# Kernel tuning notes

Hardware: AMD Instinct MI355X
Metric: run time of the kernel (lower is better)

The kernel has to match this reference:

```python
import jax, jax.numpy as jnp
import numpy as np

# module config (mirrors init_kwargs)
D_MODEL = 1024
N_HEADS = 16
HEAD_DIM = D_MODEL // N_HEADS
WINDOW = 512
PREFIX = 16
B = 2
S = 4096  # divisible by WINDOW; S > WINDOW + PREFIX -> chunked windowed path


def setup_inputs() -> dict:
    key = jax.random.key(0)
    k1, k2, k3 = jax.random.split(key, 3)
    x = jax.random.normal(k1, (B, S, D_MODEL), dtype=jnp.float32)
    w_qkv = jax.random.normal(k2, (3 * D_MODEL, D_MODEL), dtype=jnp.float32) * 0.02
    w_out = jax.random.normal(k3, (D_MODEL, D_MODEL), dtype=jnp.float32) * 0.02
    return {"x": x, "w_qkv": w_qkv, "w_out": w_out}


def _windowed_global_attention(q, k, v):
    """q,k,v: [B,H,S,Dh]. Causal sliding-window (WINDOW) + global prefix (PREFIX) attention.
    Exactly matches torch's chunked SDPA: for query chunk starting at q_start, allowed keys are
    k_pos < PREFIX (causal) plus local keys in (q_pos-WINDOW, q_pos] with k_pos >= PREFIX."""
    Bb, H, S_, Dh = q.shape
    W, P = WINDOW, PREFIX
    C = S_ // W  # number of query chunks
    scale = 1.0 / np.sqrt(Dh).astype(np.float32)

    qc = q.reshape(Bb, H, C, W, Dh)  # [B,H,C,W,Dh]
    # pad W zero-keys at front so every chunk gathers a uniform 2W-key local tail
    kp = jnp.pad(k, ((0, 0), (0, 0), (W, 0), (0, 0)))
    vp = jnp.pad(v, ((0, 0), (0, 0), (W, 0), (0, 0)))
    tail_idx = jnp.arange(C)[:, None] * W + jnp.arange(2 * W)[None, :]  # [C,2W] (padded coords)
    kt = kp[:, :, tail_idx, :]  # [B,H,C,2W,Dh]
    vt = vp[:, :, tail_idx, :]
    kg = k[:, :, :P, :]  # global prefix keys [B,H,P,Dh]
    vg = v[:, :, :P, :]

    sg = jnp.einsum('bhcqd,bhkd->bhcqk', qc, kg) * scale   # [B,H,C,W,P]
    st = jnp.einsum('bhcqd,bhckd->bhcqk', qc, kt) * scale  # [B,H,C,W,2W]

    q_pos = jnp.arange(C)[:, None] * W + jnp.arange(W)[None, :]          # [C,W]
    kt_pos = jnp.arange(C)[:, None] * W - W + jnp.arange(2 * W)[None, :]  # [C,2W]
    # global prefix: causal only
    mg = jnp.arange(P)[None, None, :] <= q_pos[:, :, None]                # [C,W,P]
    # local tail: causal & within window & not already covered by global prefix (and not padding)
    diff = q_pos[:, :, None] - kt_pos[:, None, :]                          # [C,W,2W]
    mt = (diff >= 0) & (diff < W) & (kt_pos[:, None, :] >= P)

    neg = jnp.asarray(-1e9, sg.dtype)
    scores = jnp.concatenate([
        jnp.where(mg[None, None], sg, neg),
        jnp.where(mt[None, None], st, neg),
    ], axis=-1)  # [B,H,C,W,P+2W]
    attn = jax.nn.softmax(scores, axis=-1)

    vcat = jnp.concatenate([
        jnp.broadcast_to(vg[:, :, None], (Bb, H, C, P, Dh)), vt
    ], axis=3)  # [B,H,C,P+2W,Dh]
    out = jnp.einsum('bhcqk,bhckd->bhcqd', attn, vcat)
    return out.reshape(Bb, H, S_, Dh)


def reference(x, w_qkv, w_out):
    Bb, S_, Dm = x.shape
    qkv = x @ w_qkv.T                      # [B,S,3*Dm]
    q, k, v = jnp.split(qkv, 3, axis=-1)
    def heads(t):
        return t.reshape(Bb, S_, N_HEADS, HEAD_DIM).transpose(0, 2, 1, 3)
    q, k, v = heads(q), heads(k), heads(v)  # [B,H,S,Dh]
    o = _windowed_global_attention(q, k, v)
    o = o.transpose(0, 2, 1, 3).reshape(Bb, S_, Dm)
    return o @ w_out.T
```

## Files before the change

kernel.cpp:

```cpp
#include <hip/hip_runtime.h>
#include <hip/hip_bf16.h>

#define AS1 __attribute__((address_space(1)))
#define AS3 __attribute__((address_space(3)))

typedef unsigned short u16;
typedef short bf16x8 __attribute__((ext_vector_type(8)));
typedef unsigned short u16x8 __attribute__((ext_vector_type(8)));
typedef float f32x4 __attribute__((ext_vector_type(4)));

#define MFMA16 __builtin_amdgcn_mfma_f32_16x16x32_bf16


__device__ __forceinline__ u16 f2bf(float f) {
  union { float f; unsigned u; } c; c.f = f;
  unsigned u = c.u;
  u = u + 0x7fffu + ((u >> 16) & 1u);
  return (u16)(u >> 16);
}

__device__ __forceinline__ u16 f2bf_trunc(float f) {
  union { float f; unsigned u; } c; c.f = f;
  return (u16)(c.u >> 16);
}

__device__ __forceinline__ void gl_lds16(const void* g, void* l) {
  __builtin_amdgcn_global_load_lds((const AS1 void*)g, (AS3 void*)l, 16, 0, 0);
}


__global__ void cast_all_kernel(const float* __restrict__ x,
                                const float* __restrict__ wqkv,
                                const float* __restrict__ wout,
                                u16* __restrict__ ws) {
  int i = blockIdx.x * blockDim.x + threadIdx.x;
  const float4* src;
  int rel;
  size_t matbase;
  if (i < 2097152)      { src = (const float4*)x + i;                rel = i;           matbase = 0; }
  else if (i < 2883584) { src = (const float4*)wqkv + (i - 2097152); rel = i - 2097152; matbase = 8388608; }
  else                  { src = (const float4*)wout + (i - 2883584); rel = i - 2883584; matbase = 11534336; }
  float4 f = *src;
  ushort4 o;
  o.x = f2bf(f.x); o.y = f2bf(f.y); o.z = f2bf(f.z); o.w = f2bf(f.w);
  int fe  = rel * 4;
  int row = fe >> 10, c = fe & 1023;
  int newc = (c & ~63) | (((((c >> 3) ^ row) & 7) << 3)) | (c & 7);
  ((ushort4*)ws)[(matbase + (size_t)row * 1024 + newc) >> 2] = o;
}


template<int EPI>
__global__ __launch_bounds__(256) void gemm_bt(
    const u16* __restrict__ A, const u16* __restrict__ Bm,
    float* __restrict__ Cf,
    u16* __restrict__ qd, u16* __restrict__ kd, u16* __restrict__ vd,
    int M, int N, int K)
{
  __shared__ u16 As[128 * 64];
  __shared__ u16 Bs[128 * 64];

  const int tid  = threadIdx.x;
  const int wave = tid >> 6, lane = tid & 63;
  const int quad = lane >> 4, l16 = lane & 15;
  const int bm = blockIdx.y * 128, bn = blockIdx.x * 128;
  const int wm = (wave >> 1) * 64, wn = (wave & 1) * 64;

  f32x4 acc[4][4] = {};

  const int srow = wave * 32 + (lane >> 3);
  const int scol = (lane & 7) * 8;

  for (int kt = 0; kt < K; kt += 64) {
    __syncthreads();
    #pragma unroll
    for (int i = 0; i < 4; ++i) {
      gl_lds16(&A[(size_t)(bm + srow + i * 8) * K + kt + scol], &As[(wave * 32 + i * 8) * 64]);
      gl_lds16(&Bm[(size_t)(bn + srow + i * 8) * K + kt + scol], &Bs[(wave * 32 + i * 8) * 64]);
    }
    __syncthreads();
    #pragma unroll
    for (int kk = 0; kk < 64; kk += 32) {
      bf16x8 af[4], bb[4];
      #pragma unroll
      for (int i = 0; i < 4; ++i) {
        int row = wm + i * 16 + l16;
        af[i] = *(const bf16x8*)&As[row * 64 + (((((kk >> 3) + quad) ^ row) & 7) << 3)];
      }
      #pragma unroll
      for (int j = 0; j < 4; ++j) {
        int row = wn + j * 16 + l16;
        bb[j] = *(const bf16x8*)&Bs[row * 64 + (((((kk >> 3) + quad) ^ row) & 7) << 3)];
      }
      #pragma unroll
      for (int i = 0; i < 4; ++i)
        #pragma unroll
        for (int j = 0; j < 4; ++j)
          acc[i][j] = MFMA16(af[i], bb[j], acc[i][j], 0, 0, 0);
    }
  }

  #pragma unroll
  for (int i = 0; i < 4; ++i) {
    #pragma unroll
    for (int j = 0; j < 4; ++j) {
      #pragma unroll
      for (int r = 0; r < 4; ++r) {
        int m = bm + wm + i * 16 + quad * 4 + r;
        int n = bn + wn + j * 16 + l16;
        float val = acc[i][j][r];
        if (EPI == 0) {
          Cf[(size_t)m * N + n] = val;
        } else {
          int part = n >> 10, rem = n & 1023;
          int h = rem >> 6, d = rem & 63;
          int b = m >> 12, s = m & 4095;
          if (part == 0) val *= 0.1803368801111244f;
          u16* dst = (part == 0) ? qd : (part == 1) ? kd : vd;
          dst[((size_t)((b * 16 + h) * 4096 + s)) * 64 + d] = f2bf(val);
        }
      }
    }
  }
}


__global__ __launch_bounds__(256) void transpose_v(const u16* __restrict__ vb,
                                                   u16* __restrict__ vt) {
  __shared__ u16 Lt[64 * 72];
  const int tid = threadIdx.x, bid = blockIdx.x;
  const int bh = bid & 31, st = (bid >> 5) << 6;
  const size_t base = (size_t)bh << 18;
  #pragma unroll
  for (int c = 0; c < 2; ++c) {
    int idx = tid * 8 + c * 2048;
    int row = idx >> 6, col = idx & 63;
    u16x8 vv = *(const u16x8*)&vb[base + (size_t)(st + row) * 64 + col];
    #pragma unroll
    for (int s = 0; s < 8; ++s) Lt[(col + s) * 72 + row] = vv[s];
  }
  __syncthreads();
  #pragma unroll
  for (int c = 0; c < 2; ++c) {
    int d = (tid >> 3) + c * 32;
    int sg = (tid & 7) * 8;
    u16x8 o;
    #pragma unroll
    for (int s = 0; s < 8; ++s) o[s] = Lt[d * 72 + sg + s];
    *(u16x8*)&vt[base + (size_t)d * 4096 + st + sg] = o;
  }
}


__global__ __launch_bounds__(64) void attn_kernel(
    const u16* __restrict__ qb, const u16* __restrict__ kb,
    const u16* __restrict__ vt, u16* __restrict__ ob)
{
  __shared__ u16 Ps[32 * 64];

  const int lane = threadIdx.x;
  const int quad = lane >> 4, l16 = lane & 15;
  const int bid  = blockIdx.x;
  const int bh   = bid & 31;
  const int t0   = (bid >> 5) << 5;
  const size_t base = (size_t)bh << 18;

  bf16x8 aq[2][2];
  #pragma unroll
  for (int i = 0; i < 2; ++i) {
    const u16* qrow = qb + base + (size_t)(t0 + i * 16 + l16) * 64;
    aq[i][0] = *(const bf16x8*)(qrow + quad * 8);
    aq[i][1] = *(const bf16x8*)(qrow + 32 + quad * 8);
  }

  f32x4 oacc[2][4] = {};
  f32x4 lacc[2] = {};
  bf16x8 ones;
  #pragma unroll
  for (int s = 0; s < 8; ++s) ones[s] = (short)0x3F80;

  {
    const u16* krow = kb + base + (size_t)l16 * 64;
    bf16x8 bk0 = *(const bf16x8*)(krow + quad * 8);
    bf16x8 bk1 = *(const bf16x8*)(krow + 32 + quad * 8);
    #pragma unroll
    for (int i = 0; i < 2; ++i) {
      f32x4 t4 = {};
      t4 = MFMA16(aq[i][0], bk0, t4, 0, 0, 0);
      t4 = MFMA16(aq[i][1], bk1, t4, 0, 0, 0);
      #pragma unroll
      for (int r = 0; r < 4; ++r) {
        int qpos = t0 + i * 16 + quad * 4 + r;
        float v = (l16 <= qpos) ? t4[r] : -1e30f;
        float p = exp2f(v);
        int row = i * 16 + quad * 4 + r;
        int gp = ((l16 >> 3) ^ row) & 7;
        Ps[row * 64 + (gp << 3) + (l16 & 7)] = f2bf_trunc(p);
        int gz = ((2 + (l16 >> 3)) ^ row) & 7;
        Ps[row * 64 + (gz << 3) + (l16 & 7)] = 0;
      }
    }
    bf16x8 ap[2];
    #pragma unroll
    for (int i = 0; i < 2; ++i) {
      int rowp = i * 16 + l16;
      int gb = (quad ^ rowp) & 7;
      ap[i] = *(const bf16x8*)&Ps[rowp * 64 + (gb << 3)];
      lacc[i] = MFMA16(ap[i], ones, lacc[i], 0, 0, 0);
    }
    #pragma unroll
    for (int jd = 0; jd < 4; ++jd) {
      const u16* vrow = vt + base + (size_t)(jd * 16 + l16) * 4096;
      bf16x8 bv0 = *(const bf16x8*)(vrow + quad * 8);
      #pragma unroll
      for (int i = 0; i < 2; ++i)
        oacc[i][jd] = MFMA16(ap[i], bv0, oacc[i][jd], 0, 0, 0);
    }
  }

  const int lo = max(0, t0 - 511) >> 6;
  const int hi = (t0 + 31) >> 6;

  for (int t = lo; t <= hi; ++t) {
    const int kb0 = t << 6;
    const bool full = (kb0 >= 16) && (kb0 + 63 <= t0) && (kb0 >= t0 + 31 - 511);

    #pragma unroll
    for (int j = 0; j < 4; ++j) {
      const u16* krow = kb + base + (size_t)(kb0 + j * 16 + l16) * 64;
      bf16x8 bk0 = *(const bf16x8*)(krow + quad * 8);
      bf16x8 bk1 = *(const bf16x8*)(krow + 32 + quad * 8);
      #pragma unroll
      for (int i = 0; i < 2; ++i) {
        f32x4 t4 = {};
        t4 = MFMA16(aq[i][0], bk0, t4, 0, 0, 0);
        t4 = MFMA16(aq[i][1], bk1, t4, 0, 0, 0);
        #pragma unroll
        for (int r = 0; r < 4; ++r) {
          float v = t4[r];
          if (!full) {
            int kpos = kb0 + j * 16 + l16;
            int qpos = t0 + i * 16 + quad * 4 + r;
            int diff = qpos - kpos;
            bool ok = (diff >= 0) && (diff < 512) && (kpos >= 16);
            v = ok ? v : -1e30f;
          }
          float p = exp2f(v);
          int row = i * 16 + quad * 4 + r;
          int gp = ((2 * j + (l16 >> 3)) ^ row) & 7;
          Ps[row * 64 + (gp << 3) + (l16 & 7)] = f2bf_trunc(p);
        }
      }
    }

    bf16x8 ap[2][2];
    #pragma unroll
    for (int i = 0; i < 2; ++i) {
      int rowp = i * 16 + l16;
      int gb = (quad ^ rowp) & 7;
      ap[i][0] = *(const bf16x8*)&Ps[rowp * 64 + (gb << 3)];
      ap[i][1] = *(const bf16x8*)&Ps[rowp * 64 + ((gb ^ 4) << 3)];
      lacc[i] = MFMA16(ap[i][0], ones, lacc[i], 0, 0, 0);
      lacc[i] = MFMA16(ap[i][1], ones, lacc[i], 0, 0, 0);
    }
    #pragma unroll
    for (int jd = 0; jd < 4; ++jd) {
      const u16* vrow = vt + base + (size_t)(jd * 16 + l16) * 4096 + kb0;
      bf16x8 bv0 = *(const bf16x8*)(vrow + quad * 8);
      bf16x8 bv1 = *(const bf16x8*)(vrow + 32 + quad * 8);
      #pragma unroll
      for (int i = 0; i < 2; ++i) {
        oacc[i][jd] = MFMA16(ap[i][0], bv0, oacc[i][jd], 0, 0, 0);
        oacc[i][jd] = MFMA16(ap[i][1], bv1, oacc[i][jd], 0, 0, 0);
      }
    }
  }

  const int b = bh >> 4, h = bh & 15;
  #pragma unroll
  for (int i = 0; i < 2; ++i) {
    #pragma unroll
    for (int r = 0; r < 4; ++r) {
      float inv = 1.f / lacc[i][r];
      int srow = t0 + i * 16 + quad * 4 + r;
      size_t rowoff = ((size_t)(b * 4096 + srow)) * 1024 + h * 64;
      #pragma unroll
      for (int jd = 0; jd < 4; ++jd) {
        int g = ((jd * 2 + (l16 >> 3)) ^ srow) & 7;
        ob[rowoff + (g << 3) + (l16 & 7)] = f2bf(oacc[i][jd][r] * inv);
      }
    }
  }
}


extern "C" void kernel_launch(void* const* d_in, const int* in_sizes, int n_in,
                              void* d_out, int out_size, void* d_ws, size_t ws_size,
                              hipStream_t stream) {
  const float* x    = (const float*)d_in[0];
  const float* wqkv = (const float*)d_in[1];
  const float* wout = (const float*)d_in[2];
  float* out = (float*)d_out;

  u16* ws    = (u16*)d_ws;
  u16* xb    = ws;
  u16* wqkvb = xb + (size_t)8192 * 1024;
  u16* woutb = wqkvb + (size_t)3072 * 1024;
  u16* qbuf  = woutb + (size_t)1024 * 1024;
  u16* kbuf  = qbuf + (size_t)8388608;
  u16* vbuf  = kbuf + (size_t)8388608;
  u16* vtb   = vbuf + (size_t)8388608;
  u16* obuf  = xb;

  cast_all_kernel<<<12288, 256, 0, stream>>>(x, wqkv, wout, ws);

  gemm_bt<1><<<dim3(24, 64), 256, 0, stream>>>(xb, wqkvb, nullptr, qbuf, kbuf, vbuf,
                                               8192, 3072, 1024);
  transpose_v<<<2048, 256, 0, stream>>>(vbuf, vtb);
  attn_kernel<<<4096, 64, 0, stream>>>(qbuf, kbuf, vtb, obuf);
  gemm_bt<0><<<dim3(8, 64), 256, 0, stream>>>(obuf, woutb, out, nullptr, nullptr, nullptr,
                                              8192, 1024, 1024);
}
```

Baseline: 270.3 us.

## Double-buffer K fragments and transpose QK MFMA for packed P stores

Swaps the MFMA operand order so each lane holds four consecutive key scores for one query row. That lets the probabilities be packed into 64-bit LDS stores instead of scalar 16-bit writes, with a new XOR swizzle. K fragments for the next 64-key tile are prefetched into a second register buffer while the current tile computes, to hide global load latency. This costs extra VGPRs and a manually unrolled two-tile loop.

```diff
diff --git a/kernel.cpp b/kernel.cpp
--- a/kernel.cpp
+++ b/kernel.cpp
@@ -19,14 +19,11 @@
   return (u16)(u >> 16);
 }
 
-__device__ __forceinline__ u16 f2bf_trunc(float f) {
-  union { float f; unsigned u; } c; c.f = f;
-  return (u16)(c.u >> 16);
-}
-
 __device__ __forceinline__ void gl_lds16(const void* g, void* l) {
   __builtin_amdgcn_global_load_lds((const AS1 void*)g, (AS3 void*)l, 16, 0, 0);
 }
+
+union fpu { float f; unsigned u; };
 
 
 __global__ void cast_all_kernel(const float* __restrict__ x,
@@ -165,12 +162,12 @@
   const int t0   = (bid >> 5) << 5;
   const size_t base = (size_t)bh << 18;
 
-  bf16x8 aq[2][2];
+  bf16x8 bq[2][2];
   #pragma unroll
   for (int i = 0; i < 2; ++i) {
     const u16* qrow = qb + base + (size_t)(t0 + i * 16 + l16) * 64;
-    aq[i][0] = *(const bf16x8*)(qrow + quad * 8);
-    aq[i][1] = *(const bf16x8*)(qrow + 32 + quad * 8);
+    bq[i][0] = *(const bf16x8*)(qrow + quad * 8);
+    bq[i][1] = *(const bf16x8*)(qrow + 32 + quad * 8);
   }
 
   f32x4 oacc[2][4] = {};
@@ -179,100 +176,117 @@
   #pragma unroll
   for (int s = 0; s < 8; ++s) ones[s] = (short)0x3F80;
 
+  const int lo = max(0, t0 - 511) >> 6;
+  const int hi = (t0 + 31) >> 6;
+
+  auto loadK = [&](int kb0, bf16x8 (&kf)[4][2]) {
+    #pragma unroll
+    for (int j = 0; j < 4; ++j) {
+      const u16* krow = kb + base + (size_t)(kb0 + j * 16 + l16) * 64;
+      kf[j][0] = *(const bf16x8*)(krow + quad * 8);
+      kf[j][1] = *(const bf16x8*)(krow + 32 + quad * 8);
+    }
+  };
+
+  bf16x8 ka[4][2], kbuf2[4][2];
+
   {
     const u16* krow = kb + base + (size_t)l16 * 64;
-    bf16x8 bk0 = *(const bf16x8*)(krow + quad * 8);
-    bf16x8 bk1 = *(const bf16x8*)(krow + 32 + quad * 8);
+    bf16x8 pk0 = *(const bf16x8*)(krow + quad * 8);
+    bf16x8 pk1 = *(const bf16x8*)(krow + 32 + quad * 8);
+    loadK(lo << 6, ka);
+
     #pragma unroll
     for (int i = 0; i < 2; ++i) {
       f32x4 t4 = {};
-      t4 = MFMA16(aq[i][0], bk0, t4, 0, 0, 0);
-      t4 = MFMA16(aq[i][1], bk1, t4, 0, 0, 0);
+      t4 = MFMA16(pk0, bq[i][0], t4, 0, 0, 0);
+      t4 = MFMA16(pk1, bq[i][1], t4, 0, 0, 0);
+      int row = i * 16 + l16;
+      int qpos = t0 + row;
+      fpu p[4];
       #pragma unroll
       for (int r = 0; r < 4; ++r) {
-        int qpos = t0 + i * 16 + quad * 4 + r;
-        float v = (l16 <= qpos) ? t4[r] : -1e30f;
-        float p = exp2f(v);
-        int row = i * 16 + quad * 4 + r;
-        int gp = ((l16 >> 3) ^ row) & 7;
-        Ps[row * 64 + (gp << 3) + (l16 & 7)] = f2bf_trunc(p);
-        int gz = ((2 + (l16 >> 3)) ^ row) & 7;
-        Ps[row * 64 + (gz << 3) + (l16 & 7)] = 0;
-      }
-    }
-    bf16x8 ap[2];
+        int kpos = quad * 4 + r;
+        p[r].f = exp2f(kpos <= qpos ? t4[r] : -1e30f);
+      }
+      uint2 w;
+      w.x = (p[1].u & 0xffff0000u) | (p[0].u >> 16);
+      w.y = (p[3].u & 0xffff0000u) | (p[2].u >> 16);
+      *(uint2*)&Ps[row * 64 + ((quad ^ l16) & 15) * 4] = w;
+      uint2 z = {0u, 0u};
+      *(uint2*)&Ps[row * 64 + (((4 + quad) ^ l16) & 15) * 4] = z;
+    }
     #pragma unroll
     for (int i = 0; i < 2; ++i) {
-      int rowp = i * 16 + l16;
-      int gb = (quad ^ rowp) & 7;
-      ap[i] = *(const bf16x8*)&Ps[rowp * 64 + (gb << 3)];
-      lacc[i] = MFMA16(ap[i], ones, lacc[i], 0, 0, 0);
-    }
-    #pragma unroll
-    for (int jd = 0; jd < 4; ++jd) {
-      const u16* vrow = vt + base + (size_t)(jd * 16 + l16) * 4096;
-      bf16x8 bv0 = *(const bf16x8*)(vrow + quad * 8);
-      #pragma unroll
-      for (int i = 0; i < 2; ++i)
-        oacc[i][jd] = MFMA16(ap[i], bv0, oacc[i][jd], 0, 0, 0);
-    }
-  }
-
-  const int lo = max(0, t0 - 511) >> 6;
-  const int hi = (t0 + 31) >> 6;
-
-  for (int t = lo; t <= hi; ++t) {
-    const int kb0 = t << 6;
+      int row = i * 16 + l16;
+      uint2 r0 = *(uint2*)&Ps[row * 64 + (((2 * quad) ^ l16) & 15) * 4];
+      uint2 r1 = *(uint2*)&Ps[row * 64 + (((2 * quad + 1) ^ l16) & 15) * 4];
+      union { uint4 u; bf16x8 v; } cc; cc.u = make_uint4(r0.x, r0.y, r1.x, r1.y);
+      bf16x8 ap = cc.v;
+      lacc[i] = MFMA16(ap, ones, lacc[i], 0, 0, 0);
+      #pragma unroll
+      for (int jd = 0; jd < 4; ++jd) {
+        bf16x8 bv = *(const bf16x8*)&vt[base + (size_t)(jd * 16 + l16) * 4096 + quad * 8];
+        oacc[i][jd] = MFMA16(ap, bv, oacc[i][jd], 0, 0, 0);
+      }
+    }
+  }
+
+  auto tilec = [&](int kb0, bf16x8 (&kf)[4][2]) {
     const bool full = (kb0 >= 16) && (kb0 + 63 <= t0) && (kb0 >= t0 + 31 - 511);
-
     #pragma unroll
     for (int j = 0; j < 4; ++j) {
-      const u16* krow = kb + base + (size_t)(kb0 + j * 16 + l16) * 64;
-      bf16x8 bk0 = *(const bf16x8*)(krow + quad * 8);
-      bf16x8 bk1 = *(const bf16x8*)(krow + 32 + quad * 8);
       #pragma unroll
       for (int i = 0; i < 2; ++i) {
         f32x4 t4 = {};
-        t4 = MFMA16(aq[i][0], bk0, t4, 0, 0, 0);
-        t4 = MFMA16(aq[i][1], bk1, t4, 0, 0, 0);
+        t4 = MFMA16(kf[j][0], bq[i][0], t4, 0, 0, 0);
+        t4 = MFMA16(kf[j][1], bq[i][1], t4, 0, 0, 0);
+        int row = i * 16 + l16;
+        int qpos = t0 + row;
+        fpu p[4];
         #pragma unroll
         for (int r = 0; r < 4; ++r) {
           float v = t4[r];
           if (!full) {
-            int kpos = kb0 + j * 16 + l16;
-            int qpos = t0 + i * 16 + quad * 4 + r;
+            int kpos = kb0 + j * 16 + quad * 4 + r;
             int diff = qpos - kpos;
             bool ok = (diff >= 0) && (diff < 512) && (kpos >= 16);
             v = ok ? v : -1e30f;
           }
-          float p = exp2f(v);
-          int row = i * 16 + quad * 4 + r;
-          int gp = ((2 * j + (l16 >> 3)) ^ row) & 7;
-          Ps[row * 64 + (gp << 3) + (l16 & 7)] = f2bf_trunc(p);
+          p[r].f = exp2f(v);
         }
-      }
-    }
-
-    bf16x8 ap[2][2];
+        uint2 w;
+        w.x = (p[1].u & 0xffff0000u) | (p[0].u >> 16);
+        w.y = (p[3].u & 0xffff0000u) | (p[2].u >> 16);
+        *(uint2*)&Ps[row * 64 + (((j * 4 + quad) ^ l16) & 15) * 4] = w;
+      }
+    }
     #pragma unroll
     for (int i = 0; i < 2; ++i) {
-      int rowp = i * 16 + l16;
-      int gb = (quad ^ rowp) & 7;
-      ap[i][0] = *(const bf16x8*)&Ps[rowp * 64 + (gb << 3)];
-      ap[i][1] = *(const bf16x8*)&Ps[rowp * 64 + ((gb ^ 4) << 3)];
-      lacc[i] = MFMA16(ap[i][0], ones, lacc[i], 0, 0, 0);
-      lacc[i] = MFMA16(ap[i][1], ones, lacc[i], 0, 0, 0);
-    }
-    #pragma unroll
-    for (int jd = 0; jd < 4; ++jd) {
-      const u16* vrow = vt + base + (size_t)(jd * 16 + l16) * 4096 + kb0;
-      bf16x8 bv0 = *(const bf16x8*)(vrow + quad * 8);
-      bf16x8 bv1 = *(const bf16x8*)(vrow + 32 + quad * 8);
-      #pragma unroll
-      for (int i = 0; i < 2; ++i) {
-        oacc[i][jd] = MFMA16(ap[i][0], bv0, oacc[i][jd], 0, 0, 0);
-        oacc[i][jd] = MFMA16(ap[i][1], bv1, oacc[i][jd], 0, 0, 0);
-      }
+      int row = i * 16 + l16;
+      #pragma unroll
+      for (int h = 0; h < 2; ++h) {
+        int g0 = h * 8 + 2 * quad;
+        uint2 r0 = *(uint2*)&Ps[row * 64 + ((g0 ^ l16) & 15) * 4];
+        uint2 r1 = *(uint2*)&Ps[row * 64 + (((g0 + 1) ^ l16) & 15) * 4];
+        union { uint4 u; bf16x8 v; } cc; cc.u = make_uint4(r0.x, r0.y, r1.x, r1.y);
+        bf16x8 ap = cc.v;
+        lacc[i] = MFMA16(ap, ones, lacc[i], 0, 0, 0);
+        #pragma unroll
+        for (int jd = 0; jd < 4; ++jd) {
+          bf16x8 bv = *(const bf16x8*)&vt[base + (size_t)(jd * 16 + l16) * 4096 + kb0 + h * 32 + quad * 8];
+          oacc[i][jd] = MFMA16(ap, bv, oacc[i][jd], 0, 0, 0);
+        }
+      }
+    }
+  };
+
+  for (int t = lo; t <= hi; t += 2) {
+    if (t + 1 <= hi) loadK((t + 1) << 6, kbuf2);
+    tilec(t << 6, ka);
+    if (t + 1 <= hi) {
+      if (t + 2 <= hi) loadK((t + 2) << 6, ka);
+      tilec((t + 1) << 6, kbuf2);
     }
   }
 
```

Result: no change. 265.2 us (-1.9%).
